# Optimization experiments

Hardware: AMD Instinct MI355X
Metric: run time of the kernel (lower is better)

## Reference

```python
import jax, jax.numpy as jnp
import numpy as np

B, T, C, H = 2, 2048, 2048, 16
D = C // H  # head_dim = 128
SCALE = 1.0 / np.sqrt(D)


def setup_inputs() -> dict:
    key = jax.random.key(0)
    ks = jax.random.split(key, 9)
    x = jax.random.normal(ks[0], (B, T, C), dtype=jnp.float32)
    # additive causal mask [T, T]
    attn_mask = jnp.where(jnp.tril(jnp.ones((T, T), dtype=bool)), 0.0, -1e9).astype(jnp.float32)
    s_cc = 1.0 / np.sqrt(C)
    s_cd = 1.0 / np.sqrt(C)
    Wq = jax.random.normal(ks[1], (C, C), dtype=jnp.float32) * s_cc
    Wk = jax.random.normal(ks[2], (D, C), dtype=jnp.float32) * s_cd
    Wv = jax.random.normal(ks[3], (D, C), dtype=jnp.float32) * s_cd
    Wo = jax.random.normal(ks[4], (C, C), dtype=jnp.float32) * s_cc
    bq = jnp.zeros((C,), jnp.float32)
    bk = jnp.zeros((D,), jnp.float32)
    bv = jnp.zeros((D,), jnp.float32)
    bo = jnp.zeros((C,), jnp.float32)
    return {"x": x, "attn_mask": attn_mask, "Wq": Wq, "bq": bq, "Wk": Wk,
            "bk": bk, "Wv": Wv, "bv": bv, "Wo": Wo, "bo": bo}


def reference(x, attn_mask, Wq, bq, Wk, bk, Wv, bv, Wo, bo):
    # projections (torch Linear: x @ W.T + b)
    q = (x @ Wq.T + bq).reshape(B, T, H, D).transpose(0, 2, 1, 3)  # [B,H,T,D]
    k = x @ Wk.T + bk                                              # [B,T,D] single KV head
    v = x @ Wv.T + bv                                              # [B,T,D]
    # scores: broadcast shared K over all H query heads
    scores = jnp.einsum('bhtd,bsd->bhts', q, k) * SCALE            # [B,H,T,T]
    scores = scores + attn_mask  # [T,T] broadcasts over B,H
    attn = jax.nn.softmax(scores, axis=-1)
    out = jnp.einsum('bhts,bsd->bhtd', attn, v)                    # [B,H,T,D]
    out = out.transpose(0, 2, 1, 3).reshape(B, T, C)
    return out @ Wo.T + bo
```

## Files before the change

### kernel.cpp

```cpp
#include <hip/hip_runtime.h>
#include <stdint.h>

typedef unsigned short u16;
typedef __attribute__((ext_vector_type(8))) __bf16 bf16x8;
typedef __attribute__((ext_vector_type(4))) __bf16 bf16x4;
typedef __attribute__((ext_vector_type(4))) float f32x4;
typedef __attribute__((ext_vector_type(8))) u16 u16x8;
typedef __attribute__((ext_vector_type(4))) short s16x4;
typedef __attribute__((ext_vector_type(2))) unsigned int u32x2;

#define B_SZ 2
#define T_SZ 2048
#define C_SZ 2048
#define H_SZ 16
#define D_SZ 128
#define NQKV 2304
#define ATT_SCALE 0.08838834764831845f
#define LOG2E_SCALE 0.12751744f
#define DEFER_THR 90.50967f

typedef __attribute__((address_space(1))) void* as1_void_p;
typedef __attribute__((address_space(3))) void* as3_void_p;

__device__ __forceinline__ u16 f2b(float f) {
  union { float f; uint32_t u; } c; c.f = f;
  return (u16)((c.u + 0x7FFFu + ((c.u >> 16) & 1u)) >> 16);
}

__device__ __forceinline__ void gload_lds16(const u16* g, u16* l) {
  __builtin_amdgcn_global_load_lds((as1_void_p)g, (as3_void_p)l, 16, 0, 0);
}

__device__ __forceinline__ f32x4 mfma16(s16x4 a, s16x4 b, f32x4 c) {
#if __has_builtin(__builtin_amdgcn_mfma_f32_16x16x16bf16_1k)
  return __builtin_amdgcn_mfma_f32_16x16x16bf16_1k(a, b, c, 0, 0, 0);
#elif __has_builtin(__builtin_amdgcn_mfma_f32_16x16x16_bf16)
  return __builtin_amdgcn_mfma_f32_16x16x16_bf16(
      __builtin_bit_cast(bf16x4, a), __builtin_bit_cast(bf16x4, b), c, 0, 0, 0);
#else
  u32x2 ua = __builtin_bit_cast(u32x2, a);
  u32x2 ub = __builtin_bit_cast(u32x2, b);
  asm("s_nop 1\n\tv_mfma_f32_16x16x16_bf16 %0, %1, %2, %0\n\ts_nop 7"
      : "+v"(c) : "v"(ua), "v"(ub));
  return c;
#endif
}

__global__ __launch_bounds__(256) void cast_to_bf16(const float* __restrict__ in,
                                                    u16* __restrict__ out, int n) {
  int idx = (blockIdx.x * 256 + threadIdx.x) * 4;
  if (idx >= n) return;
  float4 f = *(const float4*)&in[idx];
  ushort4 o4;
  o4.x = f2b(f.x); o4.y = f2b(f.y); o4.z = f2b(f.z); o4.w = f2b(f.w);
  *(ushort4*)&out[idx] = o4;
}

__global__ __launch_bounds__(256) void build_bias(const float* __restrict__ bq,
                                                  const float* __restrict__ bk,
                                                  const float* __restrict__ bv,
                                                  float* __restrict__ out) {
  int i = blockIdx.x * 256 + threadIdx.x;
  if (i < C_SZ) out[i] = bq[i];
  else if (i < C_SZ + D_SZ) out[i] = bk[i - C_SZ];
  else if (i < NQKV) out[i] = bv[i - C_SZ - D_SZ];
}

template <typename OutT>
__global__ __launch_bounds__(256) void gemm_bt(const u16* __restrict__ A,
                                               const u16* __restrict__ Bm,
                                               const float* __restrict__ bias,
                                               OutT* __restrict__ C,
                                               int K, int ldc) {
  __shared__ u16 lsA[2][128 * 32];
  __shared__ u16 lsB[2][128 * 32];
  const int tid = threadIdx.x;
  const int lane = tid & 63;
  const int wave = tid >> 6;
  const int wr = wave >> 1, wc = wave & 1;
  const int l16 = lane & 15, lq = lane >> 4;
  const int brow = blockIdx.y * 128;
  const int bcol = blockIdx.x * 128;

  f32x4 acc[4][4] = {};

  auto STAGE = [&](int k0, int bs) {
#pragma unroll
    for (int i = 0; i < 2; i++) {
      const int woff = (i * 4 + wave) * 512;
      const int eoff = woff + lane * 8;
      const int r = eoff >> 5, c = eoff & 31;
      gload_lds16(A + (size_t)(brow + r) * K + k0 + c, &lsA[bs][woff]);
      gload_lds16(Bm + (size_t)(bcol + r) * K + k0 + c, &lsB[bs][woff]);
    }
  };

  STAGE(0, 0);
  __syncthreads();
  int cur = 0;
  for (int k0 = 0; k0 < K; k0 += 32) {
    if (k0 + 32 < K) STAGE(k0 + 32, cur ^ 1);

    bf16x8 af[4], bfr[4];
#pragma unroll
    for (int mi = 0; mi < 4; mi++)
      af[mi] = *(const bf16x8*)&lsA[cur][(wr * 64 + mi * 16 + l16) * 32 + lq * 8];
#pragma unroll
    for (int ni = 0; ni < 4; ni++)
      bfr[ni] = *(const bf16x8*)&lsB[cur][(wc * 64 + ni * 16 + l16) * 32 + lq * 8];
#pragma unroll
    for (int mi = 0; mi < 4; mi++)
#pragma unroll
      for (int ni = 0; ni < 4; ni++)
        acc[mi][ni] = __builtin_amdgcn_mfma_f32_16x16x32_bf16(af[mi], bfr[ni], acc[mi][ni], 0, 0, 0);

    __syncthreads();
    cur ^= 1;
  }

#pragma unroll
  for (int mi = 0; mi < 4; mi++)
#pragma unroll
    for (int ni = 0; ni < 4; ni++) {
      const int col = bcol + wc * 64 + ni * 16 + l16;
      const float bb = bias ? bias[col] : 0.0f;
#pragma unroll
      for (int r = 0; r < 4; r++) {
        const int row = brow + wr * 64 + mi * 16 + lq * 4 + r;
        const float v = acc[mi][ni][r] + bb;
        if constexpr (sizeof(OutT) == 2) {
          ((u16*)C)[(size_t)row * ldc + col] = f2b(v);
        } else {
          ((float*)C)[(size_t)row * ldc + col] = v;
        }
      }
    }
}

__global__ __launch_bounds__(256) void transpose_v(const u16* __restrict__ qkv,
                                                   u16* __restrict__ vT) {
  __shared__ u16 tile[64 * 136];
  const int tid = threadIdx.x;
  const int t0 = blockIdx.x * 64;
  const int b = blockIdx.y;
#pragma unroll
  for (int i = 0; i < 4; i++) {
    int idx = (i * 256 + tid) * 8;
    int r = idx >> 7, c = idx & 127;
    u16x8 v = *(const u16x8*)&qkv[(size_t)(b * T_SZ + t0 + r) * NQKV + (C_SZ + D_SZ) + c];
    *(u16x8*)&tile[r * 136 + c] = v;
  }
  __syncthreads();
#pragma unroll
  for (int i = 0; i < 4; i++) {
    int idx = (i * 256 + tid) * 8;
    int d = idx >> 6, t = idx & 63;
    u16x8 v;
#pragma unroll
    for (int j = 0; j < 8; j++) v[j] = tile[(t + j) * 136 + d];
    *(u16x8*)&vT[(size_t)(b * D_SZ + d) * T_SZ + t0 + t] = v;
  }
}

template <bool MASK>
__device__ __forceinline__ void attn_tile64(
    const u16* lk, const u16* lv,
    const bf16x8 (&aq)[4], f32x4 (&o)[8], float& lp, float& m,
    int q_rel, int l16, int lq)
{
  f32x4 s[4] = {};
#pragma unroll
  for (int kk = 0; kk < 4; kk++) {
#pragma unroll
    for (int nb = 0; nb < 4; nb++) {
      const int row = nb * 16 + l16;
      const bf16x8 kf = *(const bf16x8*)&lk[row * 128 + (((kk * 4 + lq) ^ (row & 7)) << 3)];
      s[nb] = __builtin_amdgcn_mfma_f32_16x16x32_bf16(kf, aq[kk], s[nb], 0, 0, 0);
    }
  }
  if (MASK) {
#pragma unroll
    for (int nb = 0; nb < 4; nb++)
#pragma unroll
      for (int rr = 0; rr < 4; rr++)
        if (nb * 16 + lq * 4 + rr > q_rel) s[nb][rr] -= 1e9f;
  }
  float mx = s[0][0];
#pragma unroll
  for (int nb = 0; nb < 4; nb++)
#pragma unroll
    for (int rr = 0; rr < 4; rr++) mx = fmaxf(mx, s[nb][rr]);
  mx = fmaxf(mx, __shfl_xor(mx, 16, 64));
  mx = fmaxf(mx, __shfl_xor(mx, 32, 64));
  if (__any(mx > m + DEFER_THR)) {
    const float mnew = fmaxf(m, mx);
    const float alpha = exp2f((m - mnew) * LOG2E_SCALE);
    m = mnew;
    lp *= alpha;
#pragma unroll
    for (int nd = 0; nd < 8; nd++)
#pragma unroll
      for (int e = 0; e < 4; e++) o[nd][e] *= alpha;
  }
#pragma unroll
  for (int nb = 0; nb < 4; nb++) {
    s16x4 pb;
#pragma unroll
    for (int e = 0; e < 4; e++) {
      const float p = exp2f((s[nb][e] - m) * LOG2E_SCALE);
      lp += p;
      pb[e] = (short)f2b(p);
    }
#pragma unroll
    for (int nd = 0; nd < 8; nd++) {
      const int row = nd * 16 + l16;
      const s16x4 av = *(const s16x4*)&lv[row * 64 +
          ((((nb << 1) | (lq >> 1)) ^ (row & 7)) << 3) + ((lq & 1) << 2)];
      o[nd] = mfma16(av, pb, o[nd]);
    }
  }
}

__global__ __launch_bounds__(256, 2) void attn_fwd(const u16* __restrict__ qkv,
                                                   const u16* __restrict__ vT,
                                                   u16* __restrict__ out) {
  __shared__ u16 lsK[2][64 * 128];
  __shared__ u16 lsV[2][128 * 64];
  const int tid = threadIdx.x;
  const int w = tid >> 6, lane = tid & 63;
  const int l16 = lane & 15, lq = lane >> 4;
  const int qL = blockIdx.x;
  const int qH = 31 - qL;
  const int h = blockIdx.y;
  const int b = blockIdx.z;
  const int bT = b * T_SZ;

  bf16x8 aqL[4], aqH[4];
  {
    const size_t rL = (size_t)(bT + qL * 64 + w * 16 + l16) * NQKV + h * D_SZ;
    const size_t rH = (size_t)(bT + qH * 64 + w * 16 + l16) * NQKV + h * D_SZ;
#pragma unroll
    for (int kk = 0; kk < 4; kk++) {
      aqL[kk] = *(const bf16x8*)&qkv[rL + kk * 32 + lq * 8];
      aqH[kk] = *(const bf16x8*)&qkv[rH + kk * 32 + lq * 8];
    }
  }

  f32x4 oL[8] = {}, oH[8] = {};
  float lpL = 0.f, lpH = 0.f;
  float mL = -INFINITY, mH = -INFINITY;
  const int relDiag = w * 16 + l16;

  const u16* kp[4];
  const u16* vp[4];
#pragma unroll
  for (int j = 0; j < 4; j++) {
    const int rk = w * 16 + j * 4 + (lane >> 4);
    const int ck = (lane & 15) ^ (rk & 7);
    kp[j] = qkv + (size_t)(bT + rk) * NQKV + C_SZ + ck * 8;
    const int rv = w * 32 + j * 8 + (lane >> 3);
    const int cv = (lane & 7) ^ (rv & 7);
    vp[j] = vT + (size_t)(b * D_SZ + rv) * T_SZ + cv * 8;
  }

  auto STAGE = [&](int kt, int bufsel) {
    const size_t koff = (size_t)kt * (64 * NQKV);
    const int voff = kt * 64;
#pragma unroll
    for (int j = 0; j < 4; j++) {
      gload_lds16(kp[j] + koff, &lsK[bufsel][w * 2048 + j * 512]);
      gload_lds16(vp[j] + voff, &lsV[bufsel][w * 2048 + j * 512]);
    }
  };

  STAGE(0, 0);
  __syncthreads();
  int cur = 0;
  for (int kt = 0; kt <= qH; kt++) {
    if (kt < qH) STAGE(kt + 1, cur ^ 1);
    if (kt == qH)
      attn_tile64<true>(lsK[cur], lsV[cur], aqH, oH, lpH, mH, relDiag, l16, lq);
    else
      attn_tile64<false>(lsK[cur], lsV[cur], aqH, oH, lpH, mH, 0, l16, lq);
    if (kt == qL)
      attn_tile64<true>(lsK[cur], lsV[cur], aqL, oL, lpL, mL, relDiag, l16, lq);
    else if (kt < qL)
      attn_tile64<false>(lsK[cur], lsV[cur], aqL, oL, lpL, mL, 0, l16, lq);
    __syncthreads();
    cur ^= 1;
  }

  lpL += __shfl_xor(lpL, 16, 64); lpL += __shfl_xor(lpL, 32, 64);
  lpH += __shfl_xor(lpH, 16, 64); lpH += __shfl_xor(lpH, 32, 64);
  const float rL = __builtin_amdgcn_rcpf(lpL);
  const float rH = __builtin_amdgcn_rcpf(lpH);
  const size_t rowL = (size_t)(bT + qL * 64 + w * 16 + l16) * C_SZ + h * D_SZ;
  const size_t rowH = (size_t)(bT + qH * 64 + w * 16 + l16) * C_SZ + h * D_SZ;
#pragma unroll
  for (int nd = 0; nd < 8; nd++) {
    ushort4 sL, sH;
    sL.x = f2b(oL[nd][0] * rL); sL.y = f2b(oL[nd][1] * rL);
    sL.z = f2b(oL[nd][2] * rL); sL.w = f2b(oL[nd][3] * rL);
    sH.x = f2b(oH[nd][0] * rH); sH.y = f2b(oH[nd][1] * rH);
    sH.z = f2b(oH[nd][2] * rH); sH.w = f2b(oH[nd][3] * rH);
    *(ushort4*)&out[rowL + nd * 16 + lq * 4] = sL;
    *(ushort4*)&out[rowH + nd * 16 + lq * 4] = sH;
  }
}

extern "C" void kernel_launch(void* const* d_in, const int* in_sizes, int n_in,
                              void* d_out, int out_size, void* d_ws, size_t ws_size,
                              hipStream_t stream) {
  const float* x  = (const float*)d_in[0];
  const float* Wq = (const float*)d_in[2];
  const float* bq = (const float*)d_in[3];
  const float* Wk = (const float*)d_in[4];
  const float* bk = (const float*)d_in[5];
  const float* Wv = (const float*)d_in[6];
  const float* bv = (const float*)d_in[7];
  const float* Wo = (const float*)d_in[8];
  const float* bo = (const float*)d_in[9];
  float* out = (float*)d_out;

  char* ws = (char*)d_ws;
  if (ws_size < 71312384) return;
  u16* xb     = (u16*)(ws + 0);
  u16* wqkv   = (u16*)(ws + 16777216);
  u16* wob    = (u16*)(ws + 26214400);
  u16* qkv    = (u16*)(ws + 34603008);
  u16* vT     = (u16*)(ws + 53477376);
  u16* ao     = (u16*)(ws + 54525952);
  float* bqkv = (float*)(ws + 71303168);

  cast_to_bf16<<<8192, 256, 0, stream>>>(x, xb, 8388608);
  cast_to_bf16<<<4096, 256, 0, stream>>>(Wq, wqkv, 4194304);
  cast_to_bf16<<<256, 256, 0, stream>>>(Wk, wqkv + 4194304, 262144);
  cast_to_bf16<<<256, 256, 0, stream>>>(Wv, wqkv + 4456448, 262144);
  cast_to_bf16<<<4096, 256, 0, stream>>>(Wo, wob, 4194304);
  build_bias<<<9, 256, 0, stream>>>(bq, bk, bv, bqkv);

  gemm_bt<u16><<<dim3(18, 32), 256, 0, stream>>>(xb, wqkv, bqkv, qkv, 2048, NQKV);
  transpose_v<<<dim3(32, 2), 256, 0, stream>>>(qkv, vT);
  attn_fwd<<<dim3(16, 16, 2), 256, 0, stream>>>(qkv, vT, ao);
  gemm_bt<float><<<dim3(16, 32), 256, 0, stream>>>(ao, wob, bo, out, 2048, 2048);
}
```

Baseline: 228.0 us.

## Split attention q-tile pair across 8 waves, fuse prep kernels, remap GEMM tiles

Attention now launches 512-thread blocks where waves 0-3 handle the high q-tile and waves 4-7 the low q-tile, each keeping a single accumulator set. K uses a single LDS buffer with an extra barrier between QK and PV, and V stays double-buffered. The six cast/bias launches are merged into one prep kernel, and the GEMM workgroup index is remapped by strides of 8, presumably to group tiles for cache locality. The aim is more waves in flight and less register pressure per wave, plus fewer launches. The cost is lower-tile waves idling once past their diagonal, and an extra sync per iteration.

```diff
diff --git a/kernel.cpp b/kernel.cpp
--- a/kernel.cpp
+++ b/kernel.cpp
@@ -46,24 +46,42 @@
 #endif
 }
 
-__global__ __launch_bounds__(256) void cast_to_bf16(const float* __restrict__ in,
-                                                    u16* __restrict__ out, int n) {
-  int idx = (blockIdx.x * 256 + threadIdx.x) * 4;
-  if (idx >= n) return;
+__device__ __forceinline__ void cast4(const float* __restrict__ in,
+                                      u16* __restrict__ out, int lb, int tid) {
+  int idx = lb * 1024 + tid * 4;
   float4 f = *(const float4*)&in[idx];
   ushort4 o4;
   o4.x = f2b(f.x); o4.y = f2b(f.y); o4.z = f2b(f.z); o4.w = f2b(f.w);
   *(ushort4*)&out[idx] = o4;
 }
 
-__global__ __launch_bounds__(256) void build_bias(const float* __restrict__ bq,
-                                                  const float* __restrict__ bk,
-                                                  const float* __restrict__ bv,
-                                                  float* __restrict__ out) {
-  int i = blockIdx.x * 256 + threadIdx.x;
-  if (i < C_SZ) out[i] = bq[i];
-  else if (i < C_SZ + D_SZ) out[i] = bk[i - C_SZ];
-  else if (i < NQKV) out[i] = bv[i - C_SZ - D_SZ];
+__global__ __launch_bounds__(256) void prep(const float* __restrict__ x,
+                                            const float* __restrict__ Wq,
+                                            const float* __restrict__ Wk,
+                                            const float* __restrict__ Wv,
+                                            const float* __restrict__ Wo,
+                                            const float* __restrict__ bq,
+                                            const float* __restrict__ bk,
+                                            const float* __restrict__ bv,
+                                            u16* __restrict__ xb,
+                                            u16* __restrict__ wqkv,
+                                            u16* __restrict__ wob,
+                                            float* __restrict__ bqkv) {
+  const int bid = blockIdx.x, tid = threadIdx.x;
+  if (bid < 8192)       cast4(x,  xb,              bid,         tid);
+  else if (bid < 12288) cast4(Wq, wqkv,            bid - 8192,  tid);
+  else if (bid < 12544) cast4(Wk, wqkv + 4194304,  bid - 12288, tid);
+  else if (bid < 12800) cast4(Wv, wqkv + 4456448,  bid - 12544, tid);
+  else if (bid < 16896) cast4(Wo, wob,             bid - 12800, tid);
+  else {
+    int e = (bid - 16896) * 1024 + tid * 4;
+#pragma unroll
+    for (int j = 0; j < 4; j++) {
+      int i = e + j;
+      if (i < NQKV)
+        bqkv[i] = i < C_SZ ? bq[i] : (i < C_SZ + D_SZ ? bk[i - C_SZ] : bv[i - C_SZ - D_SZ]);
+    }
+  }
 }
 
 template <typename OutT>
@@ -79,8 +97,11 @@
   const int wave = tid >> 6;
   const int wr = wave >> 1, wc = wave & 1;
   const int l16 = lane & 15, lq = lane >> 4;
-  const int brow = blockIdx.y * 128;
-  const int bcol = blockIdx.x * 128;
+  const int nwg = gridDim.x * gridDim.y;
+  int wg = blockIdx.y * gridDim.x + blockIdx.x;
+  wg = (wg & 7) * (nwg >> 3) + (wg >> 3);
+  const int brow = (wg / gridDim.x) * 128;
+  const int bcol = (wg % gridDim.x) * 128;
 
   f32x4 acc[4][4] = {};
 
@@ -162,13 +183,8 @@
   }
 }
 
-template <bool MASK>
-__device__ __forceinline__ void attn_tile64(
-    const u16* lk, const u16* lv,
-    const bf16x8 (&aq)[4], f32x4 (&o)[8], float& lp, float& m,
-    int q_rel, int l16, int lq)
-{
-  f32x4 s[4] = {};
+__device__ __forceinline__ void qk_part(const u16* lk, const bf16x8 (&aq)[4],
+                                        f32x4 (&s)[4], int l16, int lq) {
 #pragma unroll
   for (int kk = 0; kk < 4; kk++) {
 #pragma unroll
@@ -178,7 +194,12 @@
       s[nb] = __builtin_amdgcn_mfma_f32_16x16x32_bf16(kf, aq[kk], s[nb], 0, 0, 0);
     }
   }
-  if (MASK) {
+}
+
+template <bool DIAG>
+__device__ __forceinline__ void sm_pv(const u16* lv, f32x4 (&s)[4], f32x4 (&o)[8],
+                                      float& lp, float& m, int q_rel, int l16, int lq) {
+  if (DIAG) {
 #pragma unroll
     for (int nb = 0; nb < 4; nb++)
 #pragma unroll
@@ -221,90 +242,86 @@
   }
 }
 
-__global__ __launch_bounds__(256, 2) void attn_fwd(const u16* __restrict__ qkv,
+__global__ __launch_bounds__(512, 4) void attn_fwd(const u16* __restrict__ qkv,
                                                    const u16* __restrict__ vT,
                                                    u16* __restrict__ out) {
-  __shared__ u16 lsK[2][64 * 128];
+  __shared__ u16 lsK[64 * 128];
   __shared__ u16 lsV[2][128 * 64];
   const int tid = threadIdx.x;
-  const int w = tid >> 6, lane = tid & 63;
+  const int wv = tid >> 6, lane = tid & 63;
   const int l16 = lane & 15, lq = lane >> 4;
   const int qL = blockIdx.x;
   const int qH = 31 - qL;
   const int h = blockIdx.y;
   const int b = blockIdx.z;
   const int bT = b * T_SZ;
-
-  bf16x8 aqL[4], aqH[4];
+  const int qt = (wv < 4) ? qH : qL;
+  const int wq0 = qt * 64 + (wv & 3) * 16;
+
+  bf16x8 aq[4];
   {
-    const size_t rL = (size_t)(bT + qL * 64 + w * 16 + l16) * NQKV + h * D_SZ;
-    const size_t rH = (size_t)(bT + qH * 64 + w * 16 + l16) * NQKV + h * D_SZ;
-#pragma unroll
-    for (int kk = 0; kk < 4; kk++) {
-      aqL[kk] = *(const bf16x8*)&qkv[rL + kk * 32 + lq * 8];
-      aqH[kk] = *(const bf16x8*)&qkv[rH + kk * 32 + lq * 8];
-    }
-  }
-
-  f32x4 oL[8] = {}, oH[8] = {};
-  float lpL = 0.f, lpH = 0.f;
-  float mL = -INFINITY, mH = -INFINITY;
-  const int relDiag = w * 16 + l16;
-
-  const u16* kp[4];
-  const u16* vp[4];
-#pragma unroll
-  for (int j = 0; j < 4; j++) {
-    const int rk = w * 16 + j * 4 + (lane >> 4);
-    const int ck = (lane & 15) ^ (rk & 7);
-    kp[j] = qkv + (size_t)(bT + rk) * NQKV + C_SZ + ck * 8;
-    const int rv = w * 32 + j * 8 + (lane >> 3);
-    const int cv = (lane & 7) ^ (rv & 7);
-    vp[j] = vT + (size_t)(b * D_SZ + rv) * T_SZ + cv * 8;
-  }
-
-  auto STAGE = [&](int kt, int bufsel) {
-    const size_t koff = (size_t)kt * (64 * NQKV);
-    const int voff = kt * 64;
-#pragma unroll
-    for (int j = 0; j < 4; j++) {
-      gload_lds16(kp[j] + koff, &lsK[bufsel][w * 2048 + j * 512]);
-      gload_lds16(vp[j] + voff, &lsV[bufsel][w * 2048 + j * 512]);
-    }
+    const size_t qrow = (size_t)(bT + wq0 + l16) * NQKV + h * D_SZ;
+#pragma unroll
+    for (int kk = 0; kk < 4; kk++)
+      aq[kk] = *(const bf16x8*)&qkv[qrow + kk * 32 + lq * 8];
+  }
+
+  f32x4 o[8] = {};
+  float lp = 0.f, m = -INFINITY;
+
+  const u16 *kp0, *kp1, *vp0, *vp1;
+  {
+    const int kr0 = tid >> 4,         kc0 = tid & 15;
+    const int kr1 = (512 + tid) >> 4, kc1 = tid & 15;
+    kp0 = qkv + (size_t)(bT + kr0) * NQKV + C_SZ + (size_t)((kc0 ^ (kr0 & 7)) * 8);
+    kp1 = qkv + (size_t)(bT + kr1) * NQKV + C_SZ + (size_t)((kc1 ^ (kr1 & 7)) * 8);
+    const int vr0 = tid >> 3,         vc0 = tid & 7;
+    const int vr1 = (512 + tid) >> 3, vc1 = tid & 7;
+    vp0 = vT + (size_t)(b * D_SZ + vr0) * T_SZ + (vc0 ^ (vr0 & 7)) * 8;
+    vp1 = vT + (size_t)(b * D_SZ + vr1) * T_SZ + (vc1 ^ (vr1 & 7)) * 8;
+  }
+  const int kd0 = wv * 512, kd1 = (8 + wv) * 512;
+
+  auto STAGE_K = [&](int kt) {
+    const size_t off = (size_t)kt * (64 * NQKV);
+    gload_lds16(kp0 + off, &lsK[kd0]);
+    gload_lds16(kp1 + off, &lsK[kd1]);
   };
-
-  STAGE(0, 0);
+  auto STAGE_V = [&](int kt, int bf) {
+    const int off = kt * 64;
+    gload_lds16(vp0 + off, &lsV[bf][kd0]);
+    gload_lds16(vp1 + off, &lsV[bf][kd1]);
+  };
+
+  const int nkt = qH + 1;
+  STAGE_K(0);
+  STAGE_V(0, 0);
   __syncthreads();
   int cur = 0;
-  for (int kt = 0; kt <= qH; kt++) {
-    if (kt < qH) STAGE(kt + 1, cur ^ 1);
-    if (kt == qH)
-      attn_tile64<true>(lsK[cur], lsV[cur], aqH, oH, lpH, mH, relDiag, l16, lq);
-    else
-      attn_tile64<false>(lsK[cur], lsV[cur], aqH, oH, lpH, mH, 0, l16, lq);
-    if (kt == qL)
-      attn_tile64<true>(lsK[cur], lsV[cur], aqL, oL, lpL, mL, relDiag, l16, lq);
-    else if (kt < qL)
-      attn_tile64<false>(lsK[cur], lsV[cur], aqL, oL, lpL, mL, 0, l16, lq);
+  for (int kt = 0; kt < nkt; kt++) {
+    if (kt + 1 < nkt) STAGE_V(kt + 1, cur ^ 1);
+    f32x4 s[4] = {};
+    if (kt <= qt) qk_part(lsK, aq, s, l16, lq);
+    __syncthreads();
+    if (kt + 1 < nkt) STAGE_K(kt + 1);
+    if (kt < qt)
+      sm_pv<false>(lsV[cur], s, o, lp, m, 0, l16, lq);
+    else if (kt == qt)
+      sm_pv<true>(lsV[cur], s, o, lp, m, wq0 + l16 - kt * 64, l16, lq);
     __syncthreads();
     cur ^= 1;
   }
 
-  lpL += __shfl_xor(lpL, 16, 64); lpL += __shfl_xor(lpL, 32, 64);
-  lpH += __shfl_xor(lpH, 16, 64); lpH += __shfl_xor(lpH, 32, 64);
-  const float rL = __builtin_amdgcn_rcpf(lpL);
-  const float rH = __builtin_amdgcn_rcpf(lpH);
-  const size_t rowL = (size_t)(bT + qL * 64 + w * 16 + l16) * C_SZ + h * D_SZ;
-  const size_t rowH = (size_t)(bT + qH * 64 + w * 16 + l16) * C_SZ + h * D_SZ;
+  lp += __shfl_xor(lp, 16, 64);
+  lp += __shfl_xor(lp, 32, 64);
+  const float r = __builtin_amdgcn_rcpf(lp);
+  const size_t rowb = (size_t)(bT + wq0 + l16) * C_SZ + h * D_SZ;
 #pragma unroll
   for (int nd = 0; nd < 8; nd++) {
-    ushort4 sL, sH;
-    sL.x = f2b(oL[nd][0] * rL); sL.y = f2b(oL[nd][1] * rL);
-    sL.z = f2b(oL[nd][2] * rL); sL.w = f2b(oL[nd][3] * rL);
-    sH.x = f2b(oH[nd][0] * rH); sH.y = f2b(oH[nd][1] * rH);
-    sH.z = f2b(oH[nd][2] * rH); sH.w = f2b(oH[nd][3] * rH);
-    *(ushort4*)&out[rowL + nd * 16 + lq * 4] = sL;
-    *(ushort4*)&out[rowH + nd * 16 + lq * 4] = sH;
+    ushort4 sv;
+    sv.x = f2b(o[nd][0] * r); sv.y = f2b(o[nd][1] * r);
+    sv.z = f2b(o[nd][2] * r); sv.w = f2b(o[nd][3] * r);
+    *(ushort4*)&out[rowb + nd * 16 + lq * 4] = sv;
   }
 }
 
@@ -332,15 +349,10 @@
   u16* ao     = (u16*)(ws + 54525952);
   float* bqkv = (float*)(ws + 71303168);
 
-  cast_to_bf16<<<8192, 256, 0, stream>>>(x, xb, 8388608);
-  cast_to_bf16<<<4096, 256, 0, stream>>>(Wq, wqkv, 4194304);
-  cast_to_bf16<<<256, 256, 0, stream>>>(Wk, wqkv + 4194304, 262144);
-  cast_to_bf16<<<256, 256, 0, stream>>>(Wv, wqkv + 4456448, 262144);
-  cast_to_bf16<<<4096, 256, 0, stream>>>(Wo, wob, 4194304);
-  build_bias<<<9, 256, 0, stream>>>(bq, bk, bv, bqkv);
+  prep<<<16899, 256, 0, stream>>>(x, Wq, Wk, Wv, Wo, bq, bk, bv, xb, wqkv, wob, bqkv);
 
   gemm_bt<u16><<<dim3(18, 32), 256, 0, stream>>>(xb, wqkv, bqkv, qkv, 2048, NQKV);
   transpose_v<<<dim3(32, 2), 256, 0, stream>>>(qkv, vT);
-  attn_fwd<<<dim3(16, 16, 2), 256, 0, stream>>>(qkv, vT, ao);
+  attn_fwd<<<dim3(16, 16, 2), 512, 0, stream>>>(qkv, vT, ao);
   gemm_bt<float><<<dim3(16, 32), 256, 0, stream>>>(ao, wob, bo, out, 2048, 2048);
 }
```

New measurement: 205.1 us. 10.1% less time.
